# Performance work log

Measured on AMD Instinct MI355X. Metric: run time of the kernel, lower is better.

The kernel has to match this reference:

```python
import jax, jax.numpy as jnp
import numpy as np

B, T, H, W, E, V, K = 16, 64, 16, 32, 256, 128, 3
NUM_BLOCKS = 3


def setup_inputs() -> dict:
    key = jax.random.key(0)
    ks = jax.random.split(key, 8)
    sc = 0.05  # keep logits moderate
    return {
        "encoder_output": jax.random.normal(ks[0], (B, H, W, E), jnp.float32),
        "decoder_input": jax.random.normal(ks[1], (B, H, W, E), jnp.float32),
        "labels": jax.random.randint(ks[2], (B, T), 0, V),
        "embed_table": (jax.random.normal(ks[3], (V, E), jnp.float32) * sc),
        "conv_w": (jax.random.normal(ks[4], (K, E, 2 * E), jnp.float32) * sc),  # ConvTBC weight [k, Cin, Cout]
        "conv_b": jnp.zeros((2 * E,), jnp.float32),
        "W_w": (jax.random.normal(ks[5], (E, E), jnp.float32) * sc),   # Linear(out/2 -> E), torch layout [out,in]
        "W_b": jnp.zeros((E,), jnp.float32),
        "Wo_w": (jax.random.normal(ks[6], (V, E), jnp.float32) * sc),  # Linear(E -> V)
        "Wo_b": jnp.zeros((V,), jnp.float32),
    }


def reference(encoder_output, decoder_input, embed_table, conv_w, conv_b,
              W_w, W_b, Wo_w, Wo_b, labels):
    # Work in [B, T, C]; the torch code's TBC transposes are layout-only.
    s = embed_table[labels]                     # [B, T, E]  (s in original, kept fixed)
    a = s                                       # a_l
    dec_flat = decoder_input.reshape(B, H * W, E)            # [B, HW, E]
    residual = (encoder_output + decoder_input).reshape(B, H * W, E)  # [B, HW, E]

    for _ in range(NUM_BLOCKS):
        # ConvTBC: 1D conv over T, weight [k, Cin, Cout]
        conv = jax.lax.conv_general_dilated(
            a, conv_w, window_strides=(1,), padding=((K // 2, K // 2),),
            dimension_numbers=("NWC", "WIO", "NWC")) + conv_b   # [B, T, 2E]
        # GLU over channel dim
        za, zb = jnp.split(conv, 2, axis=-1)
        z = za * jax.nn.sigmoid(zb)                              # [B, T, E]
        h = z @ W_w.T + W_b + s                                  # [B, T, E]
        # exp / sum over spatial positions == softmax over HW (same math, stable)
        scores = jnp.einsum("bte,bse->bts", h, dec_flat)         # [B, T, HW]
        alpha = jax.nn.softmax(scores, axis=2)
        # weighted sum of residual (avoids the [B,T,HW,E] repeat)
        c = jnp.einsum("bts,bse->bte", alpha, residual)          # [B, T, E]
        a = c + z

    logits = a @ Wo_w.T + Wo_b                                   # [B, T, V]
    return jax.nn.log_softmax(logits, axis=2)


if __name__ == "__main__":
    out = reference(**setup_inputs())
    print(out.shape)
```

## Files before the change

### kernel.cpp

```cpp
#include <hip/hip_runtime.h>
#include <hip/hip_bf16.h>
#include <math.h>

#define BB 16
#define TT 64
#define HWXY 512
#define EE 256
#define VV 128

typedef __bf16 bf16x8 __attribute__((ext_vector_type(8)));
typedef unsigned short u16x8 __attribute__((ext_vector_type(8)));
typedef float f32x4 __attribute__((ext_vector_type(4)));

__device__ __forceinline__ f32x4 mfma16(bf16x8 a, bf16x8 b, f32x4 c) {
    return __builtin_amdgcn_mfma_f32_16x16x32_bf16(a, b, c, 0, 0, 0);
}

__device__ __forceinline__ unsigned short f2bf(float f) {
    union { float f; unsigned int i; } v; v.f = f;
    unsigned int x = v.i;
    return (unsigned short)((x + 0x7fffu + ((x >> 16) & 1u)) >> 16);
}

__device__ __forceinline__ float bf2f(unsigned short u) {
    union { unsigned int i; float f; } v; v.i = ((unsigned int)u) << 16;
    return v.f;
}

__device__ __forceinline__ u16x8 pack8(float4 v0, float4 v1) {
    u16x8 o;
    o[0] = f2bf(v0.x); o[1] = f2bf(v0.y); o[2] = f2bf(v0.z); o[3] = f2bf(v0.w);
    o[4] = f2bf(v1.x); o[5] = f2bf(v1.y); o[6] = f2bf(v1.z); o[7] = f2bf(v1.w);
    return o;
}

__device__ __forceinline__ void dma16(const void* g, void* l) {
    __builtin_amdgcn_global_load_lds(
        (const __attribute__((address_space(1))) void*)g,
        (__attribute__((address_space(3))) void*)l, 16, 0, 0);
}

#define VMWAIT0() do { asm volatile("s_waitcnt vmcnt(0)" ::: "memory"); \
                       __builtin_amdgcn_sched_barrier(0); } while (0)

__global__ __launch_bounds__(256) void k_setup(
    const float* __restrict__ enc, const float* __restrict__ dec,
    const int* __restrict__ labels, const float* __restrict__ embed,
    const float* __restrict__ conv_w, const float* __restrict__ W_w,
    const float* __restrict__ Wo_w,
    unsigned short* __restrict__ s_bf, unsigned short* __restrict__ a_bf,
    unsigned short* __restrict__ dec_bf, unsigned short* __restrict__ resT,
    unsigned short* __restrict__ convwT, unsigned short* __restrict__ W_bf,
    unsigned short* __restrict__ Wo_bf) {
    __shared__ unsigned short tl[64][66];
    int bid = blockIdx.x;
    if (bid < 512) {
        const int b = bid >> 5, rem = bid & 31;
        const int s0 = (rem >> 2) << 6, e0 = (rem & 3) << 6;
#pragma unroll
        for (int it = 0; it < 16; ++it) {
            int lin = threadIdx.x + it * 256;
            int sl = lin >> 6, el = lin & 63;
            int src = (b * HWXY + s0 + sl) * EE + e0 + el;
            float dv = dec[src];
            dec_bf[src] = f2bf(dv);
            tl[sl][el] = f2bf(enc[src] + dv);
        }
        __syncthreads();
#pragma unroll
        for (int it = 0; it < 16; ++it) {
            int lin = threadIdx.x + it * 256;
            int el = lin >> 6, sl = lin & 63;
            resT[(b * EE + e0 + el) * HWXY + s0 + sl] = tl[sl][el];
        }
        return;
    }
    bid -= 512;
    if (bid < 96) {
        const int c0 = (bid >> 3) << 6, j0 = (bid & 7) << 6;
#pragma unroll
        for (int it = 0; it < 16; ++it) {
            int lin = threadIdx.x + it * 256;
            int cl = lin >> 6, jl = lin & 63;
            tl[cl][jl] = f2bf(conv_w[(c0 + cl) * 512 + j0 + jl]);
        }
        __syncthreads();
#pragma unroll
        for (int it = 0; it < 16; ++it) {
            int lin = threadIdx.x + it * 256;
            int jl = lin >> 6, cl = lin & 63;
            convwT[(j0 + jl) * 768 + c0 + cl] = tl[cl][jl];
        }
        return;
    }
    bid -= 96;
    int i8 = (bid * 256 + threadIdx.x) * 8;
    const int n1 = BB * TT * EE;
    const int n2 = EE * EE;
    if (i8 < n1) {
        int b = i8 >> 14, t = (i8 >> 8) & 63, e = i8 & 255;
        int lab = labels[b * TT + t];
        const float* ep = embed + lab * EE + e;
        float4 v0 = *(const float4*)ep, v1 = *(const float4*)(ep + 4);
        u16x8 p = pack8(v0, v1);
        *(u16x8*)(s_bf + i8) = p;
        *(u16x8*)(a_bf + i8) = p;
        return;
    }
    i8 -= n1;
    if (i8 < n2) {
        float4 v0 = *(const float4*)(W_w + i8), v1 = *(const float4*)(W_w + i8 + 4);
        *(u16x8*)(W_bf + i8) = pack8(v0, v1);
        return;
    }
    i8 -= n2;
    float4 v0 = *(const float4*)(Wo_w + i8), v1 = *(const float4*)(Wo_w + i8 + 4);
    *(u16x8*)(Wo_bf + i8) = pack8(v0, v1);
}

__global__ __launch_bounds__(256) void k_conv(
    const unsigned short* __restrict__ a_in, const unsigned short* __restrict__ convwT,
    const float* __restrict__ conv_b, unsigned short* __restrict__ z_bf) {
    __shared__ __align__(16) char As[33792];
    __shared__ __align__(16) char Bs[49152];
    const int ct = blockIdx.x, b = blockIdx.y;
    const int tid = threadIdx.x;
    const int w = tid >> 6, L = tid & 63, l16 = L & 15, lg = L >> 4;

#pragma unroll
    for (int i = 0; i < 12; ++i) {
        const int slot = w * 12 + i;
        const int kc = slot >> 1, half = slot & 1;
        dma16(convwT + (ct * 16 + l16 + half * 256) * 768 + kc * 32 + lg * 8,
              Bs + slot * 1024);
    }
#pragma unroll
    for (int i = 0; i < 9; ++i) {
        int unit = tid + i * 256;
        if (unit < 2112) {
            int row = unit >> 5, ch = unit & 31;
            int t = row - 1;
            u16x8 v = {0,0,0,0,0,0,0,0};
            if (t >= 0 && t < TT) v = *(const u16x8*)(a_in + (b * TT + t) * EE + ch * 8);
            *(u16x8*)(As + row * 512 + ((ch ^ (row & 7)) << 4)) = v;
        }
    }
    VMWAIT0();
    __syncthreads();

    f32x4 za = {0,0,0,0}, zb = {0,0,0,0};
#pragma unroll
    for (int kt = 0; kt < 3; ++kt) {
        const int arow = w * 16 + l16 + kt;
        const char* ab = As + arow * 512;
        const int swz = (arow & 7) << 4;
#pragma unroll
        for (int ec = 0; ec < 8; ++ec) {
            const bf16x8 af = *(const bf16x8*)(ab + ((ec * 64 + lg * 16) ^ swz));
            const int kc = kt * 8 + ec;
            za = mfma16(af, *(const bf16x8*)(Bs + (kc * 2) * 1024 + L * 16), za);
            zb = mfma16(af, *(const bf16x8*)(Bs + (kc * 2 + 1) * 1024 + L * 16), zb);
        }
    }
    const int p = ct * 16 + l16;
    const float cbA = conv_b[p], cbB = conv_b[p + 256];
#pragma unroll
    for (int j = 0; j < 4; ++j) {
        const int t = w * 16 + lg * 4 + j;
        const float v = za[j] + cbA, u = zb[j] + cbB;
        z_bf[(b * TT + t) * EE + p] = f2bf(v / (1.0f + __expf(-u)));
    }
}

__global__ __launch_bounds__(256) void k_h(
    const unsigned short* __restrict__ z_bf, const unsigned short* __restrict__ W_bf,
    const float* __restrict__ W_b, const unsigned short* __restrict__ s_bf,
    unsigned short* __restrict__ h_bf) {
    __shared__ __align__(16) char Zs[32768];
    __shared__ __align__(16) char Ws[8192];
    __shared__ unsigned short Ss[1024];
    const int ct = blockIdx.x, b = blockIdx.y;
    const int tid = threadIdx.x;
    const int w = tid >> 6, L = tid & 63, l16 = L & 15, lg = L >> 4;

#pragma unroll
    for (int i = 0; i < 8; ++i) {
        const int p = w * 8 + i;
        const int row = p * 2 + (L >> 5);
        dma16(z_bf + (b * TT + row) * EE + (((L & 31) ^ (row & 7)) << 3), Zs + p * 1024);
    }
#pragma unroll
    for (int i = 0; i < 2; ++i) {
        const int kc = w * 2 + i;
        dma16(W_bf + (ct * 16 + l16) * EE + kc * 32 + lg * 8, Ws + kc * 1024);
    }
    if (tid < 128) {
        int t = tid >> 1, part = tid & 1;
        *(u16x8*)(Ss + t * 16 + part * 8) =
            *(const u16x8*)(s_bf + (b * TT + t) * EE + ct * 16 + part * 8);
    }
    VMWAIT0();
    __syncthreads();

    f32x4 acc = {0,0,0,0};
    const int arow = w * 16 + l16;
#pragma unroll
    for (int kc = 0; kc < 8; ++kc) {
        const bf16x8 af = *(const bf16x8*)(Zs + arow * 512 + ((kc * 64 + lg * 16) ^ ((arow & 7) << 4)));
        acc = mfma16(af, *(const bf16x8*)(Ws + kc * 1024 + L * 16), acc);
    }
    const int c = ct * 16 + l16;
    const float wb = W_b[c];
#pragma unroll
    for (int j = 0; j < 4; ++j) {
        const int t = w * 16 + lg * 4 + j;
        h_bf[(b * TT + t) * EE + c] = f2bf(acc[j] + wb + bf2f(Ss[t * 16 + l16]));
    }
}

__global__ __launch_bounds__(256) void k_scores(
    const unsigned short* __restrict__ h_bf, const unsigned short* __restrict__ dec_bf,
    unsigned short* __restrict__ p_bf, float* __restrict__ m_part,
    float* __restrict__ s_part) {
    __shared__ __align__(16) char Hs[32768];
    __shared__ __align__(16) char Ds[32768];
    const int st = blockIdx.x, b = blockIdx.y;
    const int tid = threadIdx.x;
    const int w = tid >> 6, L = tid & 63, l16 = L & 15, lg = L >> 4;

#pragma unroll
    for (int i = 0; i < 8; ++i) {
        const int p = w * 8 + i;
        const int row = p * 2 + (L >> 5);
        dma16(h_bf + (b * TT + row) * EE + (((L & 31) ^ (row & 7)) << 3), Hs + p * 1024);
    }
#pragma unroll
    for (int i = 0; i < 8; ++i) {
        const int slot = w * 8 + i;
        const int kc = slot >> 2, nf = slot & 3;
        dma16(dec_bf + (b * HWXY + st * 64 + nf * 16 + l16) * EE + kc * 32 + lg * 8,
              Ds + slot * 1024);
    }
    VMWAIT0();
    __syncthreads();

    f32x4 sc[4] = {{0,0,0,0},{0,0,0,0},{0,0,0,0},{0,0,0,0}};
    const int arow = w * 16 + l16;
#pragma unroll
    for (int kc = 0; kc < 8; ++kc) {
        const bf16x8 af = *(const bf16x8*)(Hs + arow * 512 + ((kc * 64 + lg * 16) ^ ((arow & 7) << 4)));
#pragma unroll
        for (int nf = 0; nf < 4; ++nf)
            sc[nf] = mfma16(af, *(const bf16x8*)(Ds + (kc * 4 + nf) * 1024 + L * 16), sc[nf]);
    }
    float pm[4], ps[4];
#pragma unroll
    for (int j = 0; j < 4; ++j) {
        float m = fmaxf(fmaxf(sc[0][j], sc[1][j]), fmaxf(sc[2][j], sc[3][j]));
#pragma unroll
        for (int off = 8; off >= 1; off >>= 1) m = fmaxf(m, __shfl_xor(m, off));
        pm[j] = m;
        float s = 0.f;
#pragma unroll
        for (int nf = 0; nf < 4; ++nf) {
            const float pv = __expf(sc[nf][j] - m);
            sc[nf][j] = pv;
            s += pv;
        }
#pragma unroll
        for (int off = 8; off >= 1; off >>= 1) s += __shfl_xor(s, off);
        ps[j] = s;
    }
    if (l16 == 0) {
#pragma unroll
        for (int j = 0; j < 4; ++j) {
            const int t = w * 16 + lg * 4 + j;
            m_part[(b * 8 + st) * TT + t] = pm[j];
            s_part[(b * 8 + st) * TT + t] = ps[j];
        }
    }
#pragma unroll
    for (int nf = 0; nf < 4; ++nf)
#pragma unroll
        for (int j = 0; j < 4; ++j) {
            const int t = w * 16 + lg * 4 + j;
            p_bf[(b * TT + t) * HWXY + st * 64 + nf * 16 + l16] = f2bf(sc[nf][j]);
        }
}

__global__ __launch_bounds__(256) void k_attn(
    const unsigned short* __restrict__ p_bf, const unsigned short* __restrict__ resT,
    const unsigned short* __restrict__ z_bf, const float* __restrict__ m_part,
    const float* __restrict__ s_part, unsigned short* __restrict__ a_out) {
    __shared__ __align__(16) char Ps[65536];
    __shared__ __align__(16) char Bs[32768];
    __shared__ unsigned short Zr[2048];
    __shared__ float mp[512], sp[512];
    const int et = blockIdx.x, b = blockIdx.y;
    const int tid = threadIdx.x;
    const int w = tid >> 6, L = tid & 63, l16 = L & 15, lg = L >> 4;

#pragma unroll
    for (int i = 0; i < 16; ++i) {
        const int r = w * 16 + i;
        dma16(p_bf + (b * TT + r) * HWXY + ((L ^ (r & 7)) << 3), Ps + r * 1024);
    }
#pragma unroll
    for (int i = 0; i < 8; ++i) {
        const int slot = w * 8 + i;
        const int kc = slot >> 1, nf = slot & 1;
        dma16(resT + (b * EE + et * 32 + nf * 16 + l16) * HWXY + kc * 32 + lg * 8,
              Bs + slot * 1024);
    }
    {
        int t = tid >> 2, part = tid & 3;
        *(u16x8*)(Zr + t * 32 + part * 8) =
            *(const u16x8*)(z_bf + (b * TT + t) * EE + et * 32 + part * 8);
        mp[tid] = m_part[b * 512 + tid];
        mp[tid + 256] = m_part[b * 512 + tid + 256];
        sp[tid] = s_part[b * 512 + tid];
        sp[tid + 256] = s_part[b * 512 + tid + 256];
    }
    VMWAIT0();
    __syncthreads();

    float corr[4][8];
#pragma unroll
    for (int j = 0; j < 4; ++j) {
        const int t = w * 16 + lg * 4 + j;
        float mg = mp[t];
#pragma unroll
        for (int st = 1; st < 8; ++st) mg = fmaxf(mg, mp[st * 64 + t]);
        float S = 0.f;
#pragma unroll
        for (int st = 0; st < 8; ++st) {
            const float c = __expf(mp[st * 64 + t] - mg);
            corr[j][st] = c;
            S += sp[st * 64 + t] * c;
        }
        const float is = 1.0f / S;
#pragma unroll
        for (int st = 0; st < 8; ++st) corr[j][st] *= is;
    }

    f32x4 ca0 = {0,0,0,0}, ca1 = {0,0,0,0};
    const int arow = w * 16 + l16;
#pragma unroll
    for (int st = 0; st < 8; ++st) {
        f32x4 t0 = {0,0,0,0}, t1 = {0,0,0,0};
#pragma unroll
        for (int q = 0; q < 2; ++q) {
            const int kc = st * 2 + q;
            const bf16x8 af = *(const bf16x8*)(
                Ps + arow * 1024 + (((kc * 4 + lg) ^ (arow & 7)) << 4));
            t0 = mfma16(af, *(const bf16x8*)(Bs + (kc * 2) * 1024 + L * 16), t0);
            t1 = mfma16(af, *(const bf16x8*)(Bs + (kc * 2 + 1) * 1024 + L * 16), t1);
        }
#pragma unroll
        for (int j = 0; j < 4; ++j) {
            ca0[j] += t0[j] * corr[j][st];
            ca1[j] += t1[j] * corr[j][st];
        }
    }
#pragma unroll
    for (int j = 0; j < 4; ++j) {
        const int t = w * 16 + lg * 4 + j;
        unsigned short* ap = a_out + (b * TT + t) * EE + et * 32;
        ap[l16]      = f2bf(ca0[j] + bf2f(Zr[t * 32 + l16]));
        ap[l16 + 16] = f2bf(ca1[j] + bf2f(Zr[t * 32 + 16 + l16]));
    }
}

__global__ __launch_bounds__(256) void k_logits(
    const unsigned short* __restrict__ a_bf, const unsigned short* __restrict__ Wo_bf,
    const float* __restrict__ Wo_b, float* __restrict__ out) {
    __shared__ __align__(16) char As[8192];
    __shared__ __align__(16) char Ws[65536];
    __shared__ float red_m[64], red_s[64];
    const int tt = blockIdx.x, b = blockIdx.y;
    const int tid = threadIdx.x;
    const int w = tid >> 6, L = tid & 63, l16 = L & 15, lg = L >> 4;

#pragma unroll
    for (int i = 0; i < 2; ++i) {
        const int p = w * 2 + i;
        const int row = p * 2 + (L >> 5);
        dma16(a_bf + (b * TT + tt * 16 + row) * EE + (((L & 31) ^ (row & 7)) << 3),
              As + p * 1024);
    }
#pragma unroll
    for (int i = 0; i < 16; ++i) {
        const int slot = w * 16 + i;
        const int kc = slot >> 3, vg = slot & 7;
        dma16(Wo_bf + (vg * 16 + l16) * EE + kc * 32 + lg * 8, Ws + slot * 1024);
    }
    VMWAIT0();
    __syncthreads();

    f32x4 l0 = {0,0,0,0}, l1 = {0,0,0,0};
#pragma unroll
    for (int kc = 0; kc < 8; ++kc) {
        const bf16x8 af = *(const bf16x8*)(As + l16 * 512 + ((kc * 64 + lg * 16) ^ ((l16 & 7) << 4)));
        l0 = mfma16(af, *(const bf16x8*)(Ws + (kc * 8 + w * 2) * 1024 + L * 16), l0);
        l1 = mfma16(af, *(const bf16x8*)(Ws + (kc * 8 + w * 2 + 1) * 1024 + L * 16), l1);
    }
    const int v0 = w * 32 + l16, v1 = v0 + 16;
    const float wb0 = Wo_b[v0], wb1 = Wo_b[v1];
    float lv0[4], lv1[4], mg[4];
#pragma unroll
    for (int j = 0; j < 4; ++j) {
        lv0[j] = l0[j] + wb0;
        lv1[j] = l1[j] + wb1;
        float m = fmaxf(lv0[j], lv1[j]);
#pragma unroll
        for (int off = 8; off >= 1; off >>= 1) m = fmaxf(m, __shfl_xor(m, off));
        if (l16 == 0) red_m[(lg * 4 + j) * 4 + w] = m;
    }
    __syncthreads();
#pragma unroll
    for (int j = 0; j < 4; ++j) {
        const int row = lg * 4 + j;
        float m = red_m[row * 4 + 0];
#pragma unroll
        for (int ww = 1; ww < 4; ++ww) m = fmaxf(m, red_m[row * 4 + ww]);
        mg[j] = m;
        float s = __expf(lv0[j] - m) + __expf(lv1[j] - m);
#pragma unroll
        for (int off = 8; off >= 1; off >>= 1) s += __shfl_xor(s, off);
        if (l16 == 0) red_s[row * 4 + w] = s;
    }
    __syncthreads();
#pragma unroll
    for (int j = 0; j < 4; ++j) {
        const int row = lg * 4 + j;
        float s = red_s[row * 4 + 0] + red_s[row * 4 + 1] + red_s[row * 4 + 2] + red_s[row * 4 + 3];
        const float lse = mg[j] + __logf(s);
        const int gt = b * TT + tt * 16 + row;
        out[gt * VV + v0] = lv0[j] - lse;
        out[gt * VV + v1] = lv1[j] - lse;
    }
}

extern "C" void kernel_launch(void* const* d_in, const int* in_sizes, int n_in,
                              void* d_out, int out_size, void* d_ws, size_t ws_size,
                              hipStream_t stream) {
    const float* enc    = (const float*)d_in[0];
    const float* dec    = (const float*)d_in[1];
    const int*   labels = (const int*)d_in[2];
    const float* embed  = (const float*)d_in[3];
    const float* conv_w = (const float*)d_in[4];
    const float* conv_b = (const float*)d_in[5];
    const float* W_w    = (const float*)d_in[6];
    const float* W_b    = (const float*)d_in[7];
    const float* Wo_w   = (const float*)d_in[8];
    const float* Wo_b   = (const float*)d_in[9];
    float* out = (float*)d_out;
    char* ws = (char*)d_ws;

    unsigned short* a0     = (unsigned short*)(ws + 0x000000);
    unsigned short* a1     = (unsigned short*)(ws + 0x080000);
    unsigned short* s_bf   = (unsigned short*)(ws + 0x100000);
    unsigned short* dec_bf = (unsigned short*)(ws + 0x180000);
    unsigned short* resT   = (unsigned short*)(ws + 0x580000);
    unsigned short* convwT = (unsigned short*)(ws + 0x980000);
    unsigned short* W_bf   = (unsigned short*)(ws + 0xA40000);
    unsigned short* Wo_bf  = (unsigned short*)(ws + 0xA60000);
    unsigned short* z_bf   = (unsigned short*)(ws + 0xA80000);
    unsigned short* h_bf   = (unsigned short*)(ws + 0xB00000);
    unsigned short* p_bf   = (unsigned short*)(ws + 0xB80000);
    float*          m_part = (float*)(ws + 0xC80000);
    float*          s_part = (float*)(ws + 0xC88000);

    k_setup<<<784, 256, 0, stream>>>(enc, dec, labels, embed, conv_w, W_w, Wo_w,
                                     s_bf, a0, dec_bf, resT, convwT, W_bf, Wo_bf);

    unsigned short* ain = a0;
    unsigned short* aout = a1;
    for (int l = 0; l < 3; ++l) {
        k_conv<<<dim3(16, 16), 256, 0, stream>>>(ain, convwT, conv_b, z_bf);
        k_h<<<dim3(16, 16), 256, 0, stream>>>(z_bf, W_bf, W_b, s_bf, h_bf);
        k_scores<<<dim3(8, 16), 256, 0, stream>>>(h_bf, dec_bf, p_bf, m_part, s_part);
        k_attn<<<dim3(8, 16), 256, 0, stream>>>(p_bf, resT, z_bf, m_part, s_part, aout);
        unsigned short* tmp = ain; ain = aout; aout = tmp;
    }
    k_logits<<<dim3(4, 16), 256, 0, stream>>>(ain, Wo_bf, Wo_b, out);
}
```

Before: 81.24 us.

## Precompute dec·W projection to drop per-block h kernel and retile attention

Scores are rewritten as z·(dec·W) plus (s+W_b)·dec, with G = dec·W and the base term computed once in a new precompute kernel. That removes the per-block k_h launch and the h round trip. k_scores now uses 32-wide spatial tiles over 256 blocks, and k_attn splits over time into 256 blocks for more parallelism. k_conv also loads its input with async LDS DMA instead of register copies. The cost is an extra one-time GEMM over 8192 spatial rows and more global traffic for G and base_g, with some change in bf16 rounding order.

```diff
diff --git a/kernel.cpp b/kernel.cpp
--- a/kernel.cpp
+++ b/kernel.cpp
@@ -50,7 +50,7 @@
     const float* __restrict__ Wo_w,
     unsigned short* __restrict__ s_bf, unsigned short* __restrict__ a_bf,
     unsigned short* __restrict__ dec_bf, unsigned short* __restrict__ resT,
-    unsigned short* __restrict__ convwT, unsigned short* __restrict__ W_bf,
+    unsigned short* __restrict__ convwT, unsigned short* __restrict__ WT,
     unsigned short* __restrict__ Wo_bf) {
     __shared__ unsigned short tl[64][66];
     int bid = blockIdx.x;
@@ -94,9 +94,26 @@
         return;
     }
     bid -= 96;
+    if (bid < 16) {
+        const int c0 = (bid >> 2) << 6, j0 = (bid & 3) << 6;
+#pragma unroll
+        for (int it = 0; it < 16; ++it) {
+            int lin = threadIdx.x + it * 256;
+            int cl = lin >> 6, jl = lin & 63;
+            tl[cl][jl] = f2bf(W_w[(c0 + cl) * 256 + j0 + jl]);
+        }
+        __syncthreads();
+#pragma unroll
+        for (int it = 0; it < 16; ++it) {
+            int lin = threadIdx.x + it * 256;
+            int el = lin >> 6, pl = lin & 63;
+            WT[(j0 + el) * 256 + c0 + pl] = tl[pl][el];
+        }
+        return;
+    }
+    bid -= 16;
     int i8 = (bid * 256 + threadIdx.x) * 8;
     const int n1 = BB * TT * EE;
-    const int n2 = EE * EE;
     if (i8 < n1) {
         int b = i8 >> 14, t = (i8 >> 8) & 63, e = i8 & 255;
         int lab = labels[b * TT + t];
@@ -108,14 +125,102 @@
         return;
     }
     i8 -= n1;
-    if (i8 < n2) {
-        float4 v0 = *(const float4*)(W_w + i8), v1 = *(const float4*)(W_w + i8 + 4);
-        *(u16x8*)(W_bf + i8) = pack8(v0, v1);
-        return;
-    }
-    i8 -= n2;
     float4 v0 = *(const float4*)(Wo_w + i8), v1 = *(const float4*)(Wo_w + i8 + 4);
     *(u16x8*)(Wo_bf + i8) = pack8(v0, v1);
+}
+
+__global__ __launch_bounds__(256) void k_precomp(
+    const unsigned short* __restrict__ dec_bf, const unsigned short* __restrict__ WT,
+    const unsigned short* __restrict__ s_bf, const float* __restrict__ W_b,
+    unsigned short* __restrict__ G, float* __restrict__ base_g) {
+    __shared__ __align__(16) char smem[98304];
+    char* const As = smem;
+    char* const Bs = smem + 32768;
+    const int tid = threadIdx.x;
+    const int w = tid >> 6, L = tid & 63, l16 = L & 15, lg = L >> 4;
+    int bid = blockIdx.x;
+
+    if (bid < 256) {
+        const int b = bid >> 4, st = (bid >> 1) & 7, et = bid & 1;
+#pragma unroll
+        for (int i = 0; i < 8; ++i) {
+            const int p = w * 8 + i;
+            const int r = 2 * p + (L >> 5);
+            dma16(dec_bf + (b * HWXY + st * 64 + r) * EE + (((L & 31) ^ (r & 7)) << 3),
+                  As + p * 1024);
+        }
+#pragma unroll
+        for (int i = 0; i < 16; ++i) {
+            const int slot = w * 16 + i;
+            const int kc = slot >> 3, nf = slot & 7;
+            dma16(WT + (et * 128 + nf * 16 + l16) * EE + kc * 32 + lg * 8,
+                  Bs + slot * 1024);
+        }
+        VMWAIT0();
+        __syncthreads();
+        f32x4 acc[4][2] = {{{0,0,0,0},{0,0,0,0}},{{0,0,0,0},{0,0,0,0}},
+                           {{0,0,0,0},{0,0,0,0}},{{0,0,0,0},{0,0,0,0}}};
+#pragma unroll
+        for (int kc = 0; kc < 8; ++kc) {
+#pragma unroll
+            for (int m = 0; m < 4; ++m) {
+                const int arow = m * 16 + l16;
+                const bf16x8 af = *(const bf16x8*)(
+                    As + arow * 512 + (((kc * 4 + lg) ^ (arow & 7)) << 4));
+                acc[m][0] = mfma16(af, *(const bf16x8*)(Bs + (kc * 8 + w * 2) * 1024 + L * 16), acc[m][0]);
+                acc[m][1] = mfma16(af, *(const bf16x8*)(Bs + (kc * 8 + w * 2 + 1) * 1024 + L * 16), acc[m][1]);
+            }
+        }
+#pragma unroll
+        for (int m = 0; m < 4; ++m)
+#pragma unroll
+            for (int nf = 0; nf < 2; ++nf)
+#pragma unroll
+                for (int j = 0; j < 4; ++j) {
+                    const int s = st * 64 + m * 16 + lg * 4 + j;
+                    const int e = et * 128 + w * 32 + nf * 16 + l16;
+                    G[(b * HWXY + s) * EE + e] = f2bf(acc[m][nf][j]);
+                }
+    } else {
+        bid -= 256;
+        const int b = bid >> 3, st = bid & 7;
+#pragma unroll
+        for (int it = 0; it < 8; ++it) {
+            int unit = tid + it * 256;
+            int row = unit >> 5, ch = unit & 31;
+            u16x8 v = *(const u16x8*)(s_bf + (b * TT + row) * EE + ch * 8);
+            u16x8 o;
+#pragma unroll
+            for (int k = 0; k < 8; ++k) o[k] = f2bf(bf2f(v[k]) + W_b[ch * 8 + k]);
+            *(u16x8*)(As + row * 512 + ((ch ^ (row & 7)) << 4)) = o;
+        }
+#pragma unroll
+        for (int i = 0; i < 8; ++i) {
+            const int slot = w * 8 + i;
+            const int kc = slot >> 2, nf = slot & 3;
+            dma16(dec_bf + (b * HWXY + st * 64 + nf * 16 + l16) * EE + kc * 32 + lg * 8,
+                  Bs + slot * 1024);
+        }
+        VMWAIT0();
+        __syncthreads();
+        f32x4 acc[4] = {{0,0,0,0},{0,0,0,0},{0,0,0,0},{0,0,0,0}};
+        const int arow = w * 16 + l16;
+#pragma unroll
+        for (int kc = 0; kc < 8; ++kc) {
+            const bf16x8 af = *(const bf16x8*)(
+                As + arow * 512 + (((kc * 4 + lg) ^ (arow & 7)) << 4));
+#pragma unroll
+            for (int nf = 0; nf < 4; ++nf)
+                acc[nf] = mfma16(af, *(const bf16x8*)(Bs + (kc * 4 + nf) * 1024 + L * 16), acc[nf]);
+        }
+#pragma unroll
+        for (int nf = 0; nf < 4; ++nf)
+#pragma unroll
+            for (int j = 0; j < 4; ++j) {
+                const int t = w * 16 + lg * 4 + j;
+                base_g[(b * TT + t) * HWXY + st * 64 + nf * 16 + l16] = acc[nf][j];
+            }
+    }
 }
 
 __global__ __launch_bounds__(256) void k_conv(
@@ -135,15 +240,15 @@
               Bs + slot * 1024);
     }
 #pragma unroll
-    for (int i = 0; i < 9; ++i) {
-        int unit = tid + i * 256;
-        if (unit < 2112) {
-            int row = unit >> 5, ch = unit & 31;
-            int t = row - 1;
-            u16x8 v = {0,0,0,0,0,0,0,0};
-            if (t >= 0 && t < TT) v = *(const u16x8*)(a_in + (b * TT + t) * EE + ch * 8);
-            *(u16x8*)(As + row * 512 + ((ch ^ (row & 7)) << 4)) = v;
-        }
+    for (int i = 0; i < 8; ++i) {
+        const int p = w * 8 + i;
+        const int r = 1 + 2 * p + (L >> 5);
+        dma16(a_in + (b * TT + r - 1) * EE + (((L & 31) ^ (r & 7)) << 3),
+              As + 512 + p * 1024);
+    }
+    if (tid < 64) {
+        char* dst = (tid < 32) ? (As + tid * 16) : (As + 65 * 512 + (tid - 32) * 16);
+        *(u16x8*)dst = (u16x8){0,0,0,0,0,0,0,0};
     }
     VMWAIT0();
     __syncthreads();
@@ -172,58 +277,13 @@
     }
 }
 
-__global__ __launch_bounds__(256) void k_h(
-    const unsigned short* __restrict__ z_bf, const unsigned short* __restrict__ W_bf,
-    const float* __restrict__ W_b, const unsigned short* __restrict__ s_bf,
-    unsigned short* __restrict__ h_bf) {
+__global__ __launch_bounds__(256) void k_scores(
+    const unsigned short* __restrict__ z_bf, const unsigned short* __restrict__ G,
+    const float* __restrict__ base_g, unsigned short* __restrict__ p_bf,
+    float* __restrict__ m_part, float* __restrict__ s_part) {
     __shared__ __align__(16) char Zs[32768];
-    __shared__ __align__(16) char Ws[8192];
-    __shared__ unsigned short Ss[1024];
-    const int ct = blockIdx.x, b = blockIdx.y;
-    const int tid = threadIdx.x;
-    const int w = tid >> 6, L = tid & 63, l16 = L & 15, lg = L >> 4;
-
-#pragma unroll
-    for (int i = 0; i < 8; ++i) {
-        const int p = w * 8 + i;
-        const int row = p * 2 + (L >> 5);
-        dma16(z_bf + (b * TT + row) * EE + (((L & 31) ^ (row & 7)) << 3), Zs + p * 1024);
-    }
-#pragma unroll
-    for (int i = 0; i < 2; ++i) {
-        const int kc = w * 2 + i;
-        dma16(W_bf + (ct * 16 + l16) * EE + kc * 32 + lg * 8, Ws + kc * 1024);
-    }
-    if (tid < 128) {
-        int t = tid >> 1, part = tid & 1;
-        *(u16x8*)(Ss + t * 16 + part * 8) =
-            *(const u16x8*)(s_bf + (b * TT + t) * EE + ct * 16 + part * 8);
-    }
-    VMWAIT0();
-    __syncthreads();
-
-    f32x4 acc = {0,0,0,0};
-    const int arow = w * 16 + l16;
-#pragma unroll
-    for (int kc = 0; kc < 8; ++kc) {
-        const bf16x8 af = *(const bf16x8*)(Zs + arow * 512 + ((kc * 64 + lg * 16) ^ ((arow & 7) << 4)));
-        acc = mfma16(af, *(const bf16x8*)(Ws + kc * 1024 + L * 16), acc);
-    }
-    const int c = ct * 16 + l16;
-    const float wb = W_b[c];
-#pragma unroll
-    for (int j = 0; j < 4; ++j) {
-        const int t = w * 16 + lg * 4 + j;
-        h_bf[(b * TT + t) * EE + c] = f2bf(acc[j] + wb + bf2f(Ss[t * 16 + l16]));
-    }
-}
-
-__global__ __launch_bounds__(256) void k_scores(
-    const unsigned short* __restrict__ h_bf, const unsigned short* __restrict__ dec_bf,
-    unsigned short* __restrict__ p_bf, float* __restrict__ m_part,
-    float* __restrict__ s_part) {
-    __shared__ __align__(16) char Hs[32768];
-    __shared__ __align__(16) char Ds[32768];
+    __shared__ __align__(16) char Gs[16384];
+    __shared__ float basel[64 * 36];
     const int st = blockIdx.x, b = blockIdx.y;
     const int tid = threadIdx.x;
     const int w = tid >> 6, L = tid & 63, l16 = L & 15, lg = L >> 4;
@@ -231,42 +291,49 @@
 #pragma unroll
     for (int i = 0; i < 8; ++i) {
         const int p = w * 8 + i;
-        const int row = p * 2 + (L >> 5);
-        dma16(h_bf + (b * TT + row) * EE + (((L & 31) ^ (row & 7)) << 3), Hs + p * 1024);
-    }
-#pragma unroll
-    for (int i = 0; i < 8; ++i) {
-        const int slot = w * 8 + i;
-        const int kc = slot >> 2, nf = slot & 3;
-        dma16(dec_bf + (b * HWXY + st * 64 + nf * 16 + l16) * EE + kc * 32 + lg * 8,
-              Ds + slot * 1024);
+        const int r = 2 * p + (L >> 5);
+        dma16(z_bf + (b * TT + r) * EE + (((L & 31) ^ (r & 7)) << 3), Zs + p * 1024);
+    }
+#pragma unroll
+    for (int i = 0; i < 4; ++i) {
+        const int slot = w * 4 + i;
+        const int kc = slot >> 1, nf = slot & 1;
+        dma16(G + (b * HWXY + st * 32 + nf * 16 + l16) * EE + kc * 32 + lg * 8,
+              Gs + slot * 1024);
+    }
+    {
+        const int row = tid >> 2, c0 = (tid & 3) * 8;
+        const float* src = base_g + (b * TT + row) * HWXY + st * 32 + c0;
+        float4 v0 = *(const float4*)src, v1 = *(const float4*)(src + 4);
+        *(float4*)(basel + row * 36 + c0) = v0;
+        *(float4*)(basel + row * 36 + c0 + 4) = v1;
     }
     VMWAIT0();
     __syncthreads();
 
-    f32x4 sc[4] = {{0,0,0,0},{0,0,0,0},{0,0,0,0},{0,0,0,0}};
+    f32x4 sc[2] = {{0,0,0,0},{0,0,0,0}};
     const int arow = w * 16 + l16;
 #pragma unroll
     for (int kc = 0; kc < 8; ++kc) {
-        const bf16x8 af = *(const bf16x8*)(Hs + arow * 512 + ((kc * 64 + lg * 16) ^ ((arow & 7) << 4)));
-#pragma unroll
-        for (int nf = 0; nf < 4; ++nf)
-            sc[nf] = mfma16(af, *(const bf16x8*)(Ds + (kc * 4 + nf) * 1024 + L * 16), sc[nf]);
+        const bf16x8 af = *(const bf16x8*)(
+            Zs + arow * 512 + (((kc * 4 + lg) ^ (arow & 7)) << 4));
+        sc[0] = mfma16(af, *(const bf16x8*)(Gs + (kc * 2) * 1024 + L * 16), sc[0]);
+        sc[1] = mfma16(af, *(const bf16x8*)(Gs + (kc * 2 + 1) * 1024 + L * 16), sc[1]);
     }
     float pm[4], ps[4];
 #pragma unroll
     for (int j = 0; j < 4; ++j) {
-        float m = fmaxf(fmaxf(sc[0][j], sc[1][j]), fmaxf(sc[2][j], sc[3][j]));
+        const int row = w * 16 + lg * 4 + j;
+        sc[0][j] += basel[row * 36 + l16];
+        sc[1][j] += basel[row * 36 + 16 + l16];
+        float m = fmaxf(sc[0][j], sc[1][j]);
 #pragma unroll
         for (int off = 8; off >= 1; off >>= 1) m = fmaxf(m, __shfl_xor(m, off));
         pm[j] = m;
-        float s = 0.f;
-#pragma unroll
-        for (int nf = 0; nf < 4; ++nf) {
-            const float pv = __expf(sc[nf][j] - m);
-            sc[nf][j] = pv;
-            s += pv;
-        }
+        const float p0 = __expf(sc[0][j] - m);
+        const float p1 = __expf(sc[1][j] - m);
+        sc[0][j] = p0; sc[1][j] = p1;
+        float s = p0 + p1;
 #pragma unroll
         for (int off = 8; off >= 1; off >>= 1) s += __shfl_xor(s, off);
         ps[j] = s;
@@ -275,16 +342,16 @@
 #pragma unroll
         for (int j = 0; j < 4; ++j) {
             const int t = w * 16 + lg * 4 + j;
-            m_part[(b * 8 + st) * TT + t] = pm[j];
-            s_part[(b * 8 + st) * TT + t] = ps[j];
-        }
-    }
-#pragma unroll
-    for (int nf = 0; nf < 4; ++nf)
+            m_part[(b * 16 + st) * TT + t] = pm[j];
+            s_part[(b * 16 + st) * TT + t] = ps[j];
+        }
+    }
+#pragma unroll
+    for (int nf = 0; nf < 2; ++nf)
 #pragma unroll
         for (int j = 0; j < 4; ++j) {
             const int t = w * 16 + lg * 4 + j;
-            p_bf[(b * TT + t) * HWXY + st * 64 + nf * 16 + l16] = f2bf(sc[nf][j]);
+            p_bf[(b * TT + t) * HWXY + st * 32 + nf * 16 + l16] = f2bf(sc[nf][j]);
         }
 }
 
@@ -292,18 +359,18 @@
     const unsigned short* __restrict__ p_bf, const unsigned short* __restrict__ resT,
     const unsigned short* __restrict__ z_bf, const float* __restrict__ m_part,
     const float* __restrict__ s_part, unsigned short* __restrict__ a_out) {
-    __shared__ __align__(16) char Ps[65536];
+    __shared__ __align__(16) char Ps[32768];
     __shared__ __align__(16) char Bs[32768];
-    __shared__ unsigned short Zr[2048];
+    __shared__ unsigned short Zr[1024];
     __shared__ float mp[512], sp[512];
-    const int et = blockIdx.x, b = blockIdx.y;
+    const int et = blockIdx.x, tt = blockIdx.y, b = blockIdx.z;
     const int tid = threadIdx.x;
     const int w = tid >> 6, L = tid & 63, l16 = L & 15, lg = L >> 4;
 
 #pragma unroll
-    for (int i = 0; i < 16; ++i) {
-        const int r = w * 16 + i;
-        dma16(p_bf + (b * TT + r) * HWXY + ((L ^ (r & 7)) << 3), Ps + r * 1024);
+    for (int i = 0; i < 8; ++i) {
+        const int r = w * 8 + i;
+        dma16(p_bf + (b * TT + tt * 32 + r) * HWXY + ((L ^ (r & 7)) << 3), Ps + r * 1024);
     }
 #pragma unroll
     for (int i = 0; i < 8; ++i) {
@@ -313,61 +380,57 @@
               Bs + slot * 1024);
     }
     {
-        int t = tid >> 2, part = tid & 3;
-        *(u16x8*)(Zr + t * 32 + part * 8) =
-            *(const u16x8*)(z_bf + (b * TT + t) * EE + et * 32 + part * 8);
-        mp[tid] = m_part[b * 512 + tid];
-        mp[tid + 256] = m_part[b * 512 + tid + 256];
-        sp[tid] = s_part[b * 512 + tid];
-        sp[tid + 256] = s_part[b * 512 + tid + 256];
+        if (tid < 128) {
+            const int t = tid >> 2, part = tid & 3;
+            *(u16x8*)(Zr + t * 32 + part * 8) =
+                *(const u16x8*)(z_bf + (b * TT + tt * 32 + t) * EE + et * 32 + part * 8);
+        }
+        const int stl = tid >> 5, tl = tid & 31;
+        mp[tid] = m_part[(b * 16 + stl) * TT + tt * 32 + tl];
+        sp[tid] = s_part[(b * 16 + stl) * TT + tt * 32 + tl];
+        mp[tid + 256] = m_part[(b * 16 + stl + 8) * TT + tt * 32 + tl];
+        sp[tid + 256] = s_part[(b * 16 + stl + 8) * TT + tt * 32 + tl];
     }
     VMWAIT0();
     __syncthreads();
 
-    float corr[4][8];
-#pragma unroll
-    for (int j = 0; j < 4; ++j) {
-        const int t = w * 16 + lg * 4 + j;
-        float mg = mp[t];
-#pragma unroll
-        for (int st = 1; st < 8; ++st) mg = fmaxf(mg, mp[st * 64 + t]);
+    const int mg = w >> 1, nh = w & 1;
+    float corr[4][16];
+#pragma unroll
+    for (int j = 0; j < 4; ++j) {
+        const int row = mg * 16 + lg * 4 + j;
+        float mgl = mp[row];
+#pragma unroll
+        for (int s = 1; s < 16; ++s) mgl = fmaxf(mgl, mp[s * 32 + row]);
         float S = 0.f;
 #pragma unroll
-        for (int st = 0; st < 8; ++st) {
-            const float c = __expf(mp[st * 64 + t] - mg);
-            corr[j][st] = c;
-            S += sp[st * 64 + t] * c;
+        for (int s = 0; s < 16; ++s) {
+            const float c = __expf(mp[s * 32 + row] - mgl);
+            corr[j][s] = c;
+            S += sp[s * 32 + row] * c;
         }
         const float is = 1.0f / S;
 #pragma unroll
-        for (int st = 0; st < 8; ++st) corr[j][st] *= is;
-    }
-
-    f32x4 ca0 = {0,0,0,0}, ca1 = {0,0,0,0};
-    const int arow = w * 16 + l16;
-#pragma unroll
-    for (int st = 0; st < 8; ++st) {
-        f32x4 t0 = {0,0,0,0}, t1 = {0,0,0,0};
-#pragma unroll
-        for (int q = 0; q < 2; ++q) {
-            const int kc = st * 2 + q;
-            const bf16x8 af = *(const bf16x8*)(
-                Ps + arow * 1024 + (((kc * 4 + lg) ^ (arow & 7)) << 4));
-            t0 = mfma16(af, *(const bf16x8*)(Bs + (kc * 2) * 1024 + L * 16), t0);
-            t1 = mfma16(af, *(const bf16x8*)(Bs + (kc * 2 + 1) * 1024 + L * 16), t1);
-        }
-#pragma unroll
-        for (int j = 0; j < 4; ++j) {
-            ca0[j] += t0[j] * corr[j][st];
-            ca1[j] += t1[j] * corr[j][st];
-        }
-    }
-#pragma unroll
-    for (int j = 0; j < 4; ++j) {
-        const int t = w * 16 + lg * 4 + j;
-        unsigned short* ap = a_out + (b * TT + t) * EE + et * 32;
-        ap[l16]      = f2bf(ca0[j] + bf2f(Zr[t * 32 + l16]));
-        ap[l16 + 16] = f2bf(ca1[j] + bf2f(Zr[t * 32 + 16 + l16]));
+        for (int s = 0; s < 16; ++s) corr[j][s] *= is;
+    }
+
+    f32x4 ca = {0,0,0,0};
+    const int arow = mg * 16 + l16;
+#pragma unroll
+    for (int st = 0; st < 16; ++st) {
+        const bf16x8 af = *(const bf16x8*)(
+            Ps + arow * 1024 + (((st * 4 + lg) ^ (arow & 7)) << 4));
+        f32x4 t0 = mfma16(af, *(const bf16x8*)(Bs + (st * 2 + nh) * 1024 + L * 16),
+                          (f32x4){0,0,0,0});
+#pragma unroll
+        for (int j = 0; j < 4; ++j) ca[j] += t0[j] * corr[j][st];
+    }
+#pragma unroll
+    for (int j = 0; j < 4; ++j) {
+        const int row = mg * 16 + lg * 4 + j;
+        const int t = tt * 32 + row;
+        a_out[(b * TT + t) * EE + et * 32 + nh * 16 + l16] =
+            f2bf(ca[j] + bf2f(Zr[row * 32 + nh * 16 + l16]));
     }
 }
 
@@ -463,24 +526,25 @@
     unsigned short* dec_bf = (unsigned short*)(ws + 0x180000);
     unsigned short* resT   = (unsigned short*)(ws + 0x580000);
     unsigned short* convwT = (unsigned short*)(ws + 0x980000);
-    unsigned short* W_bf   = (unsigned short*)(ws + 0xA40000);
+    unsigned short* WT     = (unsigned short*)(ws + 0xA40000);
     unsigned short* Wo_bf  = (unsigned short*)(ws + 0xA60000);
     unsigned short* z_bf   = (unsigned short*)(ws + 0xA80000);
-    unsigned short* h_bf   = (unsigned short*)(ws + 0xB00000);
-    unsigned short* p_bf   = (unsigned short*)(ws + 0xB80000);
-    float*          m_part = (float*)(ws + 0xC80000);
-    float*          s_part = (float*)(ws + 0xC88000);
-
-    k_setup<<<784, 256, 0, stream>>>(enc, dec, labels, embed, conv_w, W_w, Wo_w,
-                                     s_bf, a0, dec_bf, resT, convwT, W_bf, Wo_bf);
+    unsigned short* p_bf   = (unsigned short*)(ws + 0xB00000);
+    float*          m_part = (float*)(ws + 0xC00000);
+    float*          s_part = (float*)(ws + 0xC10000);
+    float*          base_g = (float*)(ws + 0xC20000);
+    unsigned short* G      = (unsigned short*)(ws + 0xE20000);
+
+    k_setup<<<768, 256, 0, stream>>>(enc, dec, labels, embed, conv_w, W_w, Wo_w,
+                                     s_bf, a0, dec_bf, resT, convwT, WT, Wo_bf);
+    k_precomp<<<384, 256, 0, stream>>>(dec_bf, WT, s_bf, W_b, G, base_g);
 
     unsigned short* ain = a0;
     unsigned short* aout = a1;
     for (int l = 0; l < 3; ++l) {
         k_conv<<<dim3(16, 16), 256, 0, stream>>>(ain, convwT, conv_b, z_bf);
-        k_h<<<dim3(16, 16), 256, 0, stream>>>(z_bf, W_bf, W_b, s_bf, h_bf);
-        k_scores<<<dim3(8, 16), 256, 0, stream>>>(h_bf, dec_bf, p_bf, m_part, s_part);
-        k_attn<<<dim3(8, 16), 256, 0, stream>>>(p_bf, resT, z_bf, m_part, s_part, aout);
+        k_scores<<<dim3(16, 16), 256, 0, stream>>>(z_bf, G, base_g, p_bf, m_part, s_part);
+        k_attn<<<dim3(8, 2, 16), 256, 0, stream>>>(p_bf, resT, z_bf, m_part, s_part, aout);
         unsigned short* tmp = ain; ain = aout; aout = tmp;
     }
     k_logits<<<dim3(4, 16), 256, 0, stream>>>(ain, Wo_bf, Wo_b, out);
```

New measurement: 77.77 us. 1.04x faster.
